# Kernel optimization log

Hardware: AMD Instinct MI355X
Metric: run time of the kernel (lower is better)

## Reference

```python
import jax, jax.numpy as jnp
import numpy as np

T = 0.2          # temperature
W = 0.1          # loss weight
BIG = 2 ** 30    # sentinel label for masked-out samples


def setup_inputs() -> dict:
    key = jax.random.key(0)
    k1, k2, k3, k4 = jax.random.split(key, 4)
    bs, C, Gn, S = 32, 128, 256, 16
    grouped_features = jax.random.normal(k1, (bs, C, Gn, S), dtype=jnp.float32)
    # instance labels in [-1, 8): -1 = background
    proposal_instance_mask = jax.random.randint(k2, (bs, Gn, S), -1, 8, dtype=jnp.int32)
    # seed indices with duplicates possible (range 40 over 16 samples)
    grouped_indices = jax.random.randint(k3, (bs, Gn, S), 0, 40, dtype=jnp.int32)
    context_compen = jax.random.normal(k4, (1, C), dtype=jnp.float32)
    return {
        "proposal_instance_mask": proposal_instance_mask,
        "grouped_features": grouped_features,
        "grouped_indices": grouped_indices,
        "context_compen": context_compen,
    }


def _group_loss(feat, idx, lab, ctx):
    # feat: [S, C], idx: [S], lab: [S], ctx: [C]
    # NOTE: sum_{a,b} f_a . g_b / (n_f * n_g) == mean(f) . mean(g), so the
    # original tiny-mm contrastive loss reduces to pairwise dots of per-instance means.
    S, C = feat.shape
    pos = jnp.arange(S)
    # unique count of seed indices -> truncate to first u samples (as in torch code)
    si = jnp.sort(idx)
    u = 1 + jnp.sum(si[1:] != si[:-1])
    valid = pos < u
    lab_m = jnp.where(valid, lab, BIG)
    # per-group unique labels (sorted), jit-friendly
    sl = jnp.sort(lab_m)
    new = jnp.concatenate([jnp.ones((1,), bool), sl[1:] != sl[:-1]])
    cid = jnp.cumsum(new) - 1                      # compact id of each sorted label
    uniq = jnp.full((S,), BIG, sl.dtype).at[cid].set(sl)
    n_labels = jnp.sum(new & (sl != BIG))          # number of distinct valid labels
    has_bg = uniq[0] == -1                         # -1 sorts first if present
    # per-instance mean features via segment scatter-add
    comp = jnp.searchsorted(uniq, lab_m)           # sample -> compact instance slot
    sums = jnp.zeros((S, C), feat.dtype).at[comp].add(jnp.where(valid[:, None], feat, 0.0))
    cnts = jnp.zeros((S,), feat.dtype).at[comp].add(valid.astype(feat.dtype))
    means = sums / jnp.maximum(cnts, 1.0)[:, None]
    hb = has_bg.astype(jnp.int32)
    fg_count = n_labels - hb
    inst_num = fg_count + 1                        # bg slot always present
    # row 0 = bg mean (or context_compen if no bg), rows 1.. = fg means
    gidx = jnp.clip(pos + hb - 1, 0, S - 1)
    M = means[gidx]
    M = M.at[0].set(jnp.where(has_bg, M[0], ctx))
    inst_valid = pos < inst_num
    sim = (M @ M.T) / T                            # [S, S] tiny matmul of means
    sim_m = jnp.where(inst_valid[None, :], sim, -jnp.inf)
    lse = jax.scipy.special.logsumexp(sim_m, axis=1)
    li = lse - jnp.diagonal(sim)                   # -log(pos/(pos+neg)) per fg row
    fg_mask = inst_valid & (pos >= 1)
    gl = jnp.sum(jnp.where(fg_mask, li, 0.0)) / jnp.maximum(inst_num - 1, 1).astype(feat.dtype)
    return gl, fg_count >= 1


def reference(proposal_instance_mask, grouped_features, grouped_indices, context_compen):
    bs, C, Gn, S = grouped_features.shape
    feats = grouped_features.transpose(0, 2, 3, 1).reshape(-1, S, C)  # [G, S, C]
    idxs = grouped_indices.reshape(-1, S)
    labs = proposal_instance_mask.reshape(-1, S)
    ctx = context_compen[0]
    gl, gv = jax.vmap(lambda f, i, l: _group_loss(f, i, l, ctx))(feats, idxs, labs)
    gvf = gv.astype(gl.dtype)
    return jnp.sum(gl * gvf) / jnp.sum(gvf) * W
```

## Files before the change

kernel.cpp:

```cpp
#include <hip/hip_runtime.h>

#define GQ   8192
#define CCH  128
#define FSTR 20


__global__ __launch_bounds__(64, 4) void group_loss_kernel(
    const int*   __restrict__ labs,
    const float* __restrict__ feats,
    const int*   __restrict__ idxs,
    const float* __restrict__ ctx,
    float* __restrict__ ws0, float* __restrict__ ws1)
{
    __shared__ float SH[2853];
    float* F    = SH;
    float* Wm   = SH + 2560;
    float* SIMM = SH + 2740;
    float* LI   = SH + 2821;
    int*   IDXL = (int*)(SH + 2837);

    const int l   = threadIdx.x;
    const int blk = blockIdx.x;
    const int g  = ((blk & 7) << 10) | (blk >> 3);
    const int b  = g >> 8;
    const int gn = g & 255;
    const int fbase = b * (CCH * 256 * 16) + gn * 16;

    if (l < 16) IDXL[l] = idxs[g * 16 + l];
    int mylab = 0;
    if (l < 16) mylab = labs[g * 16 + l];
    __syncthreads();

    const int myidx = IDXL[l & 15];
    bool dup = false;
    #pragma unroll
    for (int j = 0; j < 15; ++j)
        dup = dup || ((j < l) && (IDXL[j] == myidx));
    const unsigned long long firstm = __ballot((l < 16) && !dup);
    const int u = __popcll(firstm);

    const bool valid = l < u;
    const int bid = valid ? (mylab + 1) : 255;

    unsigned long long memb[9];
    int cnt[9];
    #pragma unroll
    for (int r = 0; r < 9; ++r) {
        memb[r] = __ballot(bid == r);
        cnt[r]  = __popcll(memb[r]);
    }
    const bool has_bg = cnt[0] > 0;
    int fg_count = 0;
    #pragma unroll
    for (int r = 1; r < 9; ++r) fg_count += (cnt[r] > 0) ? 1 : 0;
    int pm = 0;
    #pragma unroll
    for (int r = 1; r < 9; ++r) pm |= (cnt[r] > 0) ? (1 << r) : 0;

    #pragma unroll
    for (int r = 0; r < 9; ++r) {
        float w = 0.0f;
        if (l < 16 && ((memb[r] >> l) & 1ULL)) w = 1.0f / (float)cnt[r];
        if (r == 0 && !has_bg) w = 0.0f;
        if (l < 20) Wm[r * FSTR + l] = (l < 16) ? w : 0.0f;
    }

    {
        const float* gp = feats + fbase;
        #pragma unroll
        for (int i = 0; i < 8; ++i) {
            const int c = i * 16 + (l >> 2);
            const int q = l & 3;
            float4 v = *(const float4*)(gp + c * 4096 + q * 4);
            *(float4*)(&F[c * FSTR + q * 4]) = v;
        }
    }
    __syncthreads();

    const int c0 = l, c1 = l + 64;
    float4 va[4], vb[4];
    #pragma unroll
    for (int q = 0; q < 4; ++q) {
        va[q] = *(const float4*)(&F[c0 * FSTR + q * 4]);
        vb[q] = *(const float4*)(&F[c1 * FSTR + q * 4]);
    }
    const float cx0 = ctx[c0], cx1 = ctx[c1];

    float m0[9], m1[9];
    #pragma unroll
    for (int r = 0; r < 9; ++r) {
        float a = 0.0f, c2 = 0.0f;
        #pragma unroll
        for (int q = 0; q < 4; ++q) {
            float4 w = *(const float4*)(&Wm[r * FSTR + q * 4]);
            a  += va[q].x * w.x + va[q].y * w.y + va[q].z * w.z + va[q].w * w.w;
            c2 += vb[q].x * w.x + vb[q].y * w.y + vb[q].z * w.z + vb[q].w * w.w;
        }
        m0[r] = a; m1[r] = c2;
    }
    if (!has_bg) { m0[0] = cx0; m1[0] = cx1; }

    float part[44];
    {
        int p = 0;
        #pragma unroll
        for (int i = 1; i < 9; ++i)
            #pragma unroll
            for (int j = 0; j <= i; ++j) { part[p] = m0[i] * m0[j] + m1[i] * m1[j]; ++p; }
    }
    __syncthreads();

    #pragma unroll
    for (int pass = 0; pass < 2; ++pass) {
        const int p0 = pass * 32;
        const int np = pass ? 12 : 32;
        #pragma unroll
        for (int k = 0; k < 32; ++k)
            if (k < np) F[k * 68 + l] = part[p0 + k];
        __syncthreads();
        if (l < np) {
            const int pr = p0 + l;
            const int i = (int)((sqrtf(8.0f * (float)pr + 9.0f) - 1.0f) * 0.5f);
            const int j = pr - (i * (i + 1) / 2 - 1);
            float ssum = 0.0f;
            #pragma unroll
            for (int q = 0; q < 16; ++q) {
                float4 v = *(const float4*)(&F[l * 68 + q * 4]);
                ssum += v.x + v.y + v.z + v.w;
            }
            ssum *= 5.0f;
            SIMM[i * 9 + j] = ssum;
            if (i != j) SIMM[j * 9 + i] = ssum;
        }
        __syncthreads();
    }

    float li_val = 0.0f;
    if (l >= 1 && l < 9 && ((pm >> l) & 1)) {
        float srow[9];
        #pragma unroll
        for (int j = 0; j < 9; ++j) srow[j] = SIMM[l * 9 + j];
        float vmax = srow[0];
        #pragma unroll
        for (int j = 1; j < 9; ++j)
            if ((pm >> j) & 1) vmax = fmaxf(vmax, srow[j]);
        float se = __expf(srow[0] - vmax);
        #pragma unroll
        for (int j = 1; j < 9; ++j)
            if ((pm >> j) & 1) se += __expf(srow[j] - vmax);
        const float sdiag = SIMM[l * 9 + l];
        li_val = vmax + __logf(se) - sdiag;
    }
    if (l < 9) LI[l] = li_val;
    __syncthreads();

    if (l == 0) {
        float s = 0.0f;
        #pragma unroll
        for (int r = 1; r < 9; ++r) s += LI[r];
        const float den = (float)(fg_count > 0 ? fg_count : 1);
        ws0[g] = s / den;
        ws1[g] = (fg_count > 0) ? 1.0f : 0.0f;
    }
}

__global__ __launch_bounds__(256) void reduce_kernel(
    const float* __restrict__ ws0, const float* __restrict__ ws1,
    float* __restrict__ out)
{
    __shared__ float sa[256], sb[256];
    const int t = threadIdx.x;
    float a = 0.0f, b2 = 0.0f;
    for (int g = t; g < GQ; g += 256) { a += ws0[g]; b2 += ws1[g]; }
    sa[t] = a; sb[t] = b2;
    __syncthreads();
    for (int off = 128; off > 0; off >>= 1) {
        if (t < off) { sa[t] += sa[t + off]; sb[t] += sb[t + off]; }
        __syncthreads();
    }
    if (t == 0) out[0] = 0.1f * (sa[0] / sb[0]);
}

extern "C" void kernel_launch(void* const* d_in, const int* in_sizes, int n_in,
                              void* d_out, int out_size, void* d_ws, size_t ws_size,
                              hipStream_t stream) {
    const int*   labs  = (const int*)d_in[0];
    const float* feats = (const float*)d_in[1];
    const int*   idxs  = (const int*)d_in[2];
    const float* ctx   = (const float*)d_in[3];
    float* out = (float*)d_out;
    float* ws0 = (float*)d_ws;
    float* ws1 = ws0 + GQ;

    group_loss_kernel<<<GQ, 64, 0, stream>>>(labs, feats, idxs, ctx, ws0, ws1);
    reduce_kernel<<<1, 256, 0, stream>>>(ws0, ws1, out);
}
```

Before: 121.7 us.

## Load features straight into registers and compute sims from shared means

Each thread now loads its two channel rows directly from global memory into registers, which removes the shared-memory staging of the feature tile. Label and index dedup is computed redundantly in every thread from scalar loads, replacing ballots and the weight-matrix build. Per-instance means are formed with mask-selected adds, stored to a small shared buffer, and each of the 44 pairs computes its dot product directly. This replaces the two-pass transpose reduction, and a shuffle reduction replaces the final shared-memory step. The change cuts shared memory and barriers, so occupancy can rise (launch bounds raised to 6), at the cost of more scalar and redundant per-thread work.

```diff
diff --git a/kernel.cpp b/kernel.cpp
--- a/kernel.cpp
+++ b/kernel.cpp
@@ -1,139 +1,109 @@
 #include <hip/hip_runtime.h>
 
-#define GQ   8192
-#define CCH  128
-#define FSTR 20
+#define GQ 8192
 
-
-__global__ __launch_bounds__(64, 4) void group_loss_kernel(
+__global__ __launch_bounds__(64, 6) void group_loss_kernel(
     const int*   __restrict__ labs,
     const float* __restrict__ feats,
     const int*   __restrict__ idxs,
     const float* __restrict__ ctx,
     float* __restrict__ ws0, float* __restrict__ ws1)
 {
-    __shared__ float SH[2853];
-    float* F    = SH;
-    float* Wm   = SH + 2560;
-    float* SIMM = SH + 2740;
-    float* LI   = SH + 2821;
-    int*   IDXL = (int*)(SH + 2837);
+    __shared__ float MM[9 * 132 + 4];
+    __shared__ float SIMM[81];
 
     const int l   = threadIdx.x;
     const int blk = blockIdx.x;
     const int g  = ((blk & 7) << 10) | (blk >> 3);
     const int b  = g >> 8;
     const int gn = g & 255;
-    const int fbase = b * (CCH * 256 * 16) + gn * 16;
+    const long fbase = (long)b * (128 * 256 * 16) + (long)gn * 16;
 
-    if (l < 16) IDXL[l] = idxs[g * 16 + l];
-    int mylab = 0;
-    if (l < 16) mylab = labs[g * 16 + l];
-    __syncthreads();
+    const float* gp0 = feats + fbase + (long)l * 4096;
+    const float* gp1 = gp0 + 64 * 4096;
+    float4 A[4], B[4];
+    #pragma unroll
+    for (int q = 0; q < 4; ++q) A[q] = *(const float4*)(gp0 + q * 4);
+    #pragma unroll
+    for (int q = 0; q < 4; ++q) B[q] = *(const float4*)(gp1 + q * 4);
+    const float cx0 = ctx[l], cx1 = ctx[l + 64];
 
-    const int myidx = IDXL[l & 15];
-    bool dup = false;
+    int lab_u[16], idx_u[16];
     #pragma unroll
-    for (int j = 0; j < 15; ++j)
-        dup = dup || ((j < l) && (IDXL[j] == myidx));
-    const unsigned long long firstm = __ballot((l < 16) && !dup);
-    const int u = __popcll(firstm);
-
-    const bool valid = l < u;
-    const int bid = valid ? (mylab + 1) : 255;
-
-    unsigned long long memb[9];
-    int cnt[9];
+    for (int s = 0; s < 16; ++s) {
+        lab_u[s] = labs[g * 16 + s];
+        idx_u[s] = idxs[g * 16 + s];
+    }
+    int u = 1;
+    #pragma unroll
+    for (int s = 1; s < 16; ++s) {
+        bool dup = false;
+        #pragma unroll
+        for (int j = 0; j < s; ++j) dup = dup || (idx_u[j] == idx_u[s]);
+        u += dup ? 0 : 1;
+    }
+    unsigned memb[9]; int cnt[9];
     #pragma unroll
     for (int r = 0; r < 9; ++r) {
-        memb[r] = __ballot(bid == r);
-        cnt[r]  = __popcll(memb[r]);
+        unsigned m = 0; int c = 0;
+        #pragma unroll
+        for (int s = 0; s < 16; ++s) {
+            if (s < u && lab_u[s] == r - 1) { m |= (1u << s); ++c; }
+        }
+        memb[r] = m; cnt[r] = c;
     }
     const bool has_bg = cnt[0] > 0;
-    int fg_count = 0;
+    int fg_count = 0, pm = 0;
     #pragma unroll
-    for (int r = 1; r < 9; ++r) fg_count += (cnt[r] > 0) ? 1 : 0;
-    int pm = 0;
-    #pragma unroll
-    for (int r = 1; r < 9; ++r) pm |= (cnt[r] > 0) ? (1 << r) : 0;
-
-    #pragma unroll
-    for (int r = 0; r < 9; ++r) {
-        float w = 0.0f;
-        if (l < 16 && ((memb[r] >> l) & 1ULL)) w = 1.0f / (float)cnt[r];
-        if (r == 0 && !has_bg) w = 0.0f;
-        if (l < 20) Wm[r * FSTR + l] = (l < 16) ? w : 0.0f;
+    for (int r = 1; r < 9; ++r) {
+        if (cnt[r] > 0) { ++fg_count; pm |= 1 << r; }
     }
-
-    {
-        const float* gp = feats + fbase;
-        #pragma unroll
-        for (int i = 0; i < 8; ++i) {
-            const int c = i * 16 + (l >> 2);
-            const int q = l & 3;
-            float4 v = *(const float4*)(gp + c * 4096 + q * 4);
-            *(float4*)(&F[c * FSTR + q * 4]) = v;
-        }
-    }
-    __syncthreads();
-
-    const int c0 = l, c1 = l + 64;
-    float4 va[4], vb[4];
-    #pragma unroll
-    for (int q = 0; q < 4; ++q) {
-        va[q] = *(const float4*)(&F[c0 * FSTR + q * 4]);
-        vb[q] = *(const float4*)(&F[c1 * FSTR + q * 4]);
-    }
-    const float cx0 = ctx[c0], cx1 = ctx[c1];
 
     float m0[9], m1[9];
     #pragma unroll
     for (int r = 0; r < 9; ++r) {
-        float a = 0.0f, c2 = 0.0f;
+        float a = 0.0f, bb = 0.0f;
+        const unsigned m = memb[r];
         #pragma unroll
         for (int q = 0; q < 4; ++q) {
-            float4 w = *(const float4*)(&Wm[r * FSTR + q * 4]);
-            a  += va[q].x * w.x + va[q].y * w.y + va[q].z * w.z + va[q].w * w.w;
-            c2 += vb[q].x * w.x + vb[q].y * w.y + vb[q].z * w.z + vb[q].w * w.w;
+            if (m & (1u << (4 * q + 0))) { a += A[q].x; bb += B[q].x; }
+            if (m & (1u << (4 * q + 1))) { a += A[q].y; bb += B[q].y; }
+            if (m & (1u << (4 * q + 2))) { a += A[q].z; bb += B[q].z; }
+            if (m & (1u << (4 * q + 3))) { a += A[q].w; bb += B[q].w; }
         }
-        m0[r] = a; m1[r] = c2;
+        const float invc = 1.0f / (float)(cnt[r] > 0 ? cnt[r] : 1);
+        m0[r] = a * invc;
+        m1[r] = bb * invc;
     }
     if (!has_bg) { m0[0] = cx0; m1[0] = cx1; }
 
-    float part[44];
-    {
-        int p = 0;
-        #pragma unroll
-        for (int i = 1; i < 9; ++i)
-            #pragma unroll
-            for (int j = 0; j <= i; ++j) { part[p] = m0[i] * m0[j] + m1[i] * m1[j]; ++p; }
+    #pragma unroll
+    for (int r = 0; r < 9; ++r) {
+        MM[r * 132 + l]      = m0[r];
+        MM[r * 132 + 64 + l] = m1[r];
     }
     __syncthreads();
 
-    #pragma unroll
-    for (int pass = 0; pass < 2; ++pass) {
-        const int p0 = pass * 32;
-        const int np = pass ? 12 : 32;
+    float simv = 0.0f; int pi = 0, pj = 0;
+    if (l < 44) {
+        pi = (int)((sqrtf(8.0f * (float)l + 9.0f) - 1.0f) * 0.5f);
+        pj = l - (pi * (pi + 1) / 2 - 1);
+        const float* Ri = MM + pi * 132;
+        const float* Rj = MM + pj * 132;
+        float acc = 0.0f;
         #pragma unroll
-        for (int k = 0; k < 32; ++k)
-            if (k < np) F[k * 68 + l] = part[p0 + k];
-        __syncthreads();
-        if (l < np) {
-            const int pr = p0 + l;
-            const int i = (int)((sqrtf(8.0f * (float)pr + 9.0f) - 1.0f) * 0.5f);
-            const int j = pr - (i * (i + 1) / 2 - 1);
-            float ssum = 0.0f;
-            #pragma unroll
-            for (int q = 0; q < 16; ++q) {
-                float4 v = *(const float4*)(&F[l * 68 + q * 4]);
-                ssum += v.x + v.y + v.z + v.w;
-            }
-            ssum *= 5.0f;
-            SIMM[i * 9 + j] = ssum;
-            if (i != j) SIMM[j * 9 + i] = ssum;
+        for (int q = 0; q < 32; ++q) {
+            float4 x = *(const float4*)(Ri + 4 * q);
+            float4 y = *(const float4*)(Rj + 4 * q);
+            acc += x.x * y.x + x.y * y.y + x.z * y.z + x.w * y.w;
         }
-        __syncthreads();
+        simv = acc * 5.0f;
     }
+    if (l < 44) {
+        SIMM[pi * 9 + pj] = simv;
+        if (pi != pj) SIMM[pj * 9 + pi] = simv;
+    }
+    __syncthreads();
 
     float li_val = 0.0f;
     if (l >= 1 && l < 9 && ((pm >> l) & 1)) {
@@ -148,18 +118,14 @@
         #pragma unroll
         for (int j = 1; j < 9; ++j)
             if ((pm >> j) & 1) se += __expf(srow[j] - vmax);
-        const float sdiag = SIMM[l * 9 + l];
-        li_val = vmax + __logf(se) - sdiag;
+        li_val = vmax + __logf(se) - srow[l];
     }
-    if (l < 9) LI[l] = li_val;
-    __syncthreads();
 
+    float ssum = li_val;
+    #pragma unroll
+    for (int off = 8; off >= 1; off >>= 1) ssum += __shfl_down(ssum, off);
     if (l == 0) {
-        float s = 0.0f;
-        #pragma unroll
-        for (int r = 1; r < 9; ++r) s += LI[r];
-        const float den = (float)(fg_count > 0 ? fg_count : 1);
-        ws0[g] = s / den;
+        ws0[g] = ssum / (float)(fg_count > 0 ? fg_count : 1);
         ws1[g] = (fg_count > 0) ? 1.0f : 0.0f;
     }
 }
```

After: 129.2 us. 6.1% more time.
